# Performance work log

Hardware: AMD Instinct MI355X
Metric: run time of the kernel (lower is better)

Reference implementation:

```python
import jax, jax.numpy as jnp
import numpy as np

B, S, D, H, E, HID = 4, 1024, 768, 12, 8, 3072
DH = D // H

def _ln(x, g, b, eps=1e-5):
    m = jnp.mean(x, -1, keepdims=True)
    v = jnp.mean((x - m) ** 2, -1, keepdims=True)
    return (x - m) * jax.lax.rsqrt(v + eps) * g + b

def setup_inputs():
    key = jax.random.key(0)
    ks = jax.random.split(key, 16)
    p = lambda k, s: jax.random.normal(k, s, jnp.float32) * 0.02
    causal = jnp.triu(jnp.ones((S, S), bool), 1)  # True = masked (future)
    return {
        "x": jax.random.normal(ks[0], (B, S, D), jnp.float32),
        "mask": jnp.broadcast_to(causal, (B, S, S)),
        "ln_attn_g": jnp.ones((D,), jnp.float32), "ln_attn_b": jnp.zeros((D,), jnp.float32),
        "wq": p(ks[1], (D, D)), "bq": jnp.zeros((D,), jnp.float32),
        "wk": p(ks[2], (D, D)), "bk": jnp.zeros((D,), jnp.float32),
        "wv": p(ks[3], (D, D)), "bv": jnp.zeros((D,), jnp.float32),
        "wo": p(ks[4], (D, D)), "bo": jnp.zeros((D,), jnp.float32),
        "ln_ff_g": jnp.ones((D,), jnp.float32), "ln_ff_b": jnp.zeros((D,), jnp.float32),
        "gate_w": p(ks[5], (D, E)), "gate_b": jnp.zeros((E,), jnp.float32),
        "w1": p(ks[6], (E, D, HID)), "b1": jnp.zeros((E, HID), jnp.float32),
        "w2": p(ks[7], (E, HID, D)), "b2": jnp.zeros((E, D), jnp.float32),
        "moe_ln_g": jnp.ones((D,), jnp.float32), "moe_ln_b": jnp.zeros((D,), jnp.float32),
        "top_k": 2,
    }

def reference(x, mask, ln_attn_g, ln_attn_b, wq, bq, wk, bk, wv, bv, wo, bo,
              ln_ff_g, ln_ff_b, gate_w, gate_b, w1, b1, w2, b2,
              moe_ln_g, moe_ln_b, top_k):
    # --- pre-LN multi-head self-attention + residual ---
    a = _ln(x, ln_attn_g, ln_attn_b)
    q = (a @ wq + bq).reshape(B, S, H, DH)
    k = (a @ wk + bk).reshape(B, S, H, DH)
    v = (a @ wv + bv).reshape(B, S, H, DH)
    scores = jnp.einsum("bqhd,bkhd->bhqk", q, k) / jnp.sqrt(jnp.float32(DH))
    scores = jnp.where(mask[:, None, :, :], jnp.float32(-1e9), scores)
    probs = jax.nn.softmax(scores, axis=-1)
    ctx = jnp.einsum("bhqk,bkhd->bqhd", probs, v).reshape(B, S, D)
    x = x + (ctx @ wo + bo)
    # --- MoE positionwise FF (CustomizedMoEPositionwiseFF, pre_lnorm=False) ---
    h = _ln(x, ln_ff_g, ln_ff_b)                        # ln_ff(x) fed into ff
    logits = h @ gate_w + gate_b                        # [B,S,E] naive gate
    vals, idx = jax.lax.top_k(logits, top_k)            # [B,S,k]
    sc = jax.nn.softmax(vals, axis=-1)                  # softmax over top-k logits
    # dense all-expert compute (dropless reference for dispatch+grouped GEMM)
    e1 = jax.nn.relu(jnp.einsum("bsd,edh->bseh", h, w1) + b1)  # [B,S,E,HID]
    e2 = jnp.einsum("bseh,ehd->bsed", e1, w2) + b2             # [B,S,E,D]
    sel = jnp.take_along_axis(e2, idx[..., None], axis=2)      # [B,S,k,D]
    core = jnp.sum(sel * sc[..., None], axis=2)                # combine
    moe_out = _ln(h + core, moe_ln_g, moe_ln_b)                # post-lnorm
    return x + moe_out
```

## Files before the change

### kernel.cpp

```cpp
#include <hip/hip_runtime.h>
#include <hip/hip_bf16.h>
#include <stdint.h>

using bf16 = __hip_bfloat16;
typedef short s16x8 __attribute__((ext_vector_type(8)));
typedef float f32x4 __attribute__((ext_vector_type(4)));

#define NB 4
#define NS 1024
#define ND 768
#define NH 12
#define NE 8
#define NHID 3072
#define NTOK 4096
#define NASSIGN 8192
#define MAXCH 72
#define MAXSLOT (MAXCH * 128)

__device__ __forceinline__ float bf2f(bf16 v){ return __bfloat162float(v); }
__device__ __forceinline__ bf16 f2bf(float v){ return __float2bfloat16(v); }

__device__ __forceinline__ void gload_lds16(const bf16* g, bf16* l){
  __builtin_amdgcn_global_load_lds((const __attribute__((address_space(1))) void*)g,
                                   (__attribute__((address_space(3))) void*)l, 16, 0, 0);
}

__global__ void transpose_convert_kernel(const float* __restrict__ src, bf16* __restrict__ dst,
                                         int K, int N){
  __shared__ float tile[32][33];
  int bz = blockIdx.z;
  src += (size_t)bz * K * N;
  dst += (size_t)bz * N * K;
  int n0 = blockIdx.x * 32, k0 = blockIdx.y * 32;
  int tx = threadIdx.x & 31, ty = threadIdx.x >> 5;
  #pragma unroll
  for (int i = 0; i < 4; i++){
    int k = ty + i * 8;
    tile[k][tx] = src[(size_t)(k0 + k) * N + n0 + tx];
  }
  __syncthreads();
  #pragma unroll
  for (int i = 0; i < 4; i++){
    int n = ty + i * 8;
    dst[(size_t)(n0 + n) * K + k0 + tx] = f2bf(tile[tx][n]);
  }
}

__global__ void concat3_kernel(const float* __restrict__ a, const float* __restrict__ b,
                               const float* __restrict__ c, float* __restrict__ out){
  int i = blockIdx.x * 256 + threadIdx.x;
  if (i >= 3 * ND) return;
  float v = (i < ND) ? a[i] : (i < 2 * ND ? b[i - ND] : c[i - 2 * ND]);
  out[i] = v;
}

template<bool OF, bool OB>
__global__ void ln_kernel(const float* __restrict__ in, const float* __restrict__ g,
                          const float* __restrict__ bb, float* __restrict__ of,
                          bf16* __restrict__ ob){
  int row = blockIdx.x, t = threadIdx.x;
  const float* x = in + (size_t)row * ND;
  float v[3]; float s = 0.f, sq = 0.f;
  #pragma unroll
  for (int i = 0; i < 3; i++){ v[i] = x[t + i * 256]; s += v[i]; sq += v[i] * v[i]; }
  __shared__ float rs[4], rq[4];
  #pragma unroll
  for (int d = 32; d >= 1; d >>= 1){ s += __shfl_xor(s, d); sq += __shfl_xor(sq, d); }
  int w = t >> 6;
  if ((t & 63) == 0){ rs[w] = s; rq[w] = sq; }
  __syncthreads();
  s = rs[0] + rs[1] + rs[2] + rs[3];
  sq = rq[0] + rq[1] + rq[2] + rq[3];
  float mean = s * (1.f / ND);
  float var = sq * (1.f / ND) - mean * mean;
  float rstd = rsqrtf(var + 1e-5f);
  #pragma unroll
  for (int i = 0; i < 3; i++){
    int idx = t + i * 256;
    float y = (v[i] - mean) * rstd * g[idx] + bb[idx];
    if (OF) of[(size_t)row * ND + idx] = y;
    if (OB) ob[(size_t)row * ND + idx] = f2bf(y);
  }
}

template<int GROUP, bool GATHER, bool RELU, bool OBF, bool RESID, bool SEG>
__global__ __launch_bounds__(256, 3)
void gemm_kernel(const bf16* __restrict__ A, int ldA,
                 const bf16* __restrict__ BtB,
                 const float* __restrict__ biasB,
                 void* __restrict__ Cv, int ldC,
                 const float* __restrict__ resid,
                 int N, int K,
                 const int* __restrict__ chunk_e, const int* __restrict__ tok){
  __shared__ __align__(16) bf16 sA[2][128 * 32];
  __shared__ __align__(16) bf16 sB[2][128 * 32];

  int t = threadIdx.x;
  int lane = t & 63, wv = t >> 6;
  int c0i = wv * 128 + lane;
  int r0  = c0i >> 2;
  int kk  = (c0i & 3) * 8;
  int nt = blockIdx.x;
  int wm = (wv >> 1) * 64, wn = (wv & 1) * 64;
  int l16 = lane & 15, q4 = lane >> 4;
  int aoff[4], boff[4];
  #pragma unroll
  for (int mi = 0; mi < 4; mi++) aoff[mi] = (wm + mi * 16 + l16) * 32 + q4 * 8;
  #pragma unroll
  for (int ni = 0; ni < 4; ni++) boff[ni] = (wn + ni * 16 + l16) * 32 + q4 * 8;

  for (int g = 0; g < GROUP; g++){
    int c = blockIdx.y * GROUP + g;
    int e = 0;
    if (SEG){ e = chunk_e[c]; if (e < 0) break; }
    const bf16* Bt = SEG ? BtB + (size_t)e * N * K : BtB;
    const float* bias = SEG ? biasB + (size_t)e * N : biasB;
    size_t arow0, arow1;
    int m0 = c * 128 + r0, m1 = m0 + 16;
    if (GATHER){ arow0 = (size_t)tok[m0]; arow1 = (size_t)tok[m1]; }
    else       { arow0 = (size_t)m0;      arow1 = (size_t)m1; }
    const bf16* gA0 = A + arow0 * ldA + kk;
    const bf16* gA1 = A + arow1 * ldA + kk;
    const bf16* gB0 = Bt + (size_t)(nt * 128 + r0) * K + kk;
    const bf16* gB1 = Bt + (size_t)(nt * 128 + r0 + 16) * K + kk;

    if (g > 0) __syncthreads();

    f32x4 acc[4][4] = {};
    gload_lds16(gA0, &sA[0][(size_t)c0i * 8]);
    gload_lds16(gA1, &sA[0][(size_t)(c0i + 64) * 8]);
    gload_lds16(gB0, &sB[0][(size_t)c0i * 8]);
    gload_lds16(gB1, &sB[0][(size_t)(c0i + 64) * 8]);

    int nk = K >> 5;
    for (int ki = 0; ki < nk; ki++){
      int cur = ki & 1;
      __syncthreads();
      if (ki + 1 < nk){
        int nxt = cur ^ 1, off = (ki + 1) * 32;
        gload_lds16(gA0 + off, &sA[nxt][(size_t)c0i * 8]);
        gload_lds16(gA1 + off, &sA[nxt][(size_t)(c0i + 64) * 8]);
        gload_lds16(gB0 + off, &sB[nxt][(size_t)c0i * 8]);
        gload_lds16(gB1 + off, &sB[nxt][(size_t)(c0i + 64) * 8]);
      }
      s16x8 af[4], bfr[4];
      #pragma unroll
      for (int mi = 0; mi < 4; mi++) af[mi] = *(const s16x8*)(&sA[cur][0] + aoff[mi]);
      #pragma unroll
      for (int ni = 0; ni < 4; ni++) bfr[ni] = *(const s16x8*)(&sB[cur][0] + boff[ni]);
      #pragma unroll
      for (int mi = 0; mi < 4; mi++)
        #pragma unroll
        for (int ni = 0; ni < 4; ni++)
          acc[mi][ni] = __builtin_amdgcn_mfma_f32_16x16x32_bf16(af[mi], bfr[ni], acc[mi][ni], 0, 0, 0);
    }

    #pragma unroll
    for (int mi = 0; mi < 4; mi++){
      #pragma unroll
      for (int ni = 0; ni < 4; ni++){
        int col = nt * 128 + wn + ni * 16 + l16;
        float bv = bias[col];
        #pragma unroll
        for (int r = 0; r < 4; r++){
          size_t crow = (size_t)(c * 128 + wm + mi * 16 + q4 * 4 + r);
          float v = acc[mi][ni][r] + bv;
          if (RELU) v = fmaxf(v, 0.f);
          if (RESID) v += resid[crow * ldC + col];
          if (OBF) ((bf16*)Cv)[crow * ldC + col] = f2bf(v);
          else     ((float*)Cv)[crow * ldC + col] = v;
        }
      }
    }
  }
}

__global__ void vtrans_kernel(const bf16* __restrict__ qkv, bf16* __restrict__ vT){
  __shared__ bf16 tile[32][33];
  int bh = blockIdx.z; int b = bh / NH, h = bh % NH;
  int s0 = blockIdx.x * 32, d0 = blockIdx.y * 32;
  int tx = threadIdx.x & 31, ty = threadIdx.x >> 5;
  #pragma unroll
  for (int i = 0; i < 4; i++){
    int s = s0 + ty + i * 8;
    tile[ty + i * 8][tx] = qkv[(size_t)(b * NS + s) * 2304 + 1536 + h * 64 + d0 + tx];
  }
  __syncthreads();
  #pragma unroll
  for (int i = 0; i < 4; i++){
    int d = ty + i * 8;
    vT[((size_t)bh * 64 + d0 + d) * NS + s0 + tx] = tile[tx][d];
  }
}

#define SPAD 72
__global__ __launch_bounds__(256, 3)
void flash_attn_kernel(const bf16* __restrict__ qkv, const bf16* __restrict__ vT,
                       bf16* __restrict__ ctx){
  __shared__ __align__(16) bf16 sP[4][16 * SPAD];
  int qt = blockIdx.x, h = blockIdx.y, b = blockIdx.z;
  int t = threadIdx.x, lane = t & 63, wv = t >> 6;
  int l16 = lane & 15, q4 = lane >> 4;
  int q0 = qt * 64 + wv * 16;
  const size_t ldq = 2304;
  const bf16* qbase = qkv + (size_t)(b * NS) * ldq + h * 64;
  const bf16* kbase = qbase + 768;
  const bf16* vtb = vT + (size_t)(b * NH + h) * 64 * NS;
  bf16* sPw = &sP[wv][0];
  const f32x4 fzero = {0.f, 0.f, 0.f, 0.f};

  s16x8 qf[2];
  #pragma unroll
  for (int kh = 0; kh < 2; kh++)
    qf[kh] = *(const s16x8*)(qbase + (size_t)(q0 + l16) * ldq + kh * 32 + q4 * 8);

  f32x4 O[4] = {};
  float ms[4], ls[4];
  #pragma unroll
  for (int r = 0; r < 4; r++){ ms[r] = -1e30f; ls[r] = 0.f; }

  int kend = q0 + 16;
  for (int key0 = 0; key0 < kend; key0 += 64){
    s16x8 kf[4][2];
    #pragma unroll
    for (int ni = 0; ni < 4; ni++)
      #pragma unroll
      for (int kh = 0; kh < 2; kh++)
        kf[ni][kh] = *(const s16x8*)(kbase + (size_t)(key0 + ni * 16 + l16) * ldq + kh * 32 + q4 * 8);
    f32x4 Sf[4];
    #pragma unroll
    for (int ni = 0; ni < 4; ni++){
      Sf[ni] = __builtin_amdgcn_mfma_f32_16x16x32_bf16(qf[0], kf[ni][0], fzero, 0, 0, 0);
      Sf[ni] = __builtin_amdgcn_mfma_f32_16x16x32_bf16(qf[1], kf[ni][1], Sf[ni], 0, 0, 0);
    }
    s16x8 vf[4][2];
    #pragma unroll
    for (int dt = 0; dt < 4; dt++)
      #pragma unroll
      for (int kh = 0; kh < 2; kh++)
        vf[dt][kh] = *(const s16x8*)(vtb + (size_t)(dt * 16 + l16) * NS + key0 + kh * 32 + q4 * 8);

    bool need_mask = (key0 + 63 >= q0);
    #pragma unroll
    for (int r = 0; r < 4; r++){
      int qrow = q0 + q4 * 4 + r;
      float sv[4];
      #pragma unroll
      for (int ni = 0; ni < 4; ni++){
        sv[ni] = Sf[ni][r] * 0.125f;
        if (need_mask && (key0 + ni * 16 + l16 > qrow)) sv[ni] = -1e30f;
      }
      float mx = fmaxf(fmaxf(sv[0], sv[1]), fmaxf(sv[2], sv[3]));
      #pragma unroll
      for (int d = 8; d >= 1; d >>= 1) mx = fmaxf(mx, __shfl_xor(mx, d));
      float mnew = fmaxf(ms[r], mx);
      float alpha = __expf(ms[r] - mnew);
      float p[4], psum = 0.f;
      #pragma unroll
      for (int ni = 0; ni < 4; ni++){ p[ni] = __expf(sv[ni] - mnew); psum += p[ni]; }
      #pragma unroll
      for (int d = 8; d >= 1; d >>= 1) psum += __shfl_xor(psum, d);
      ls[r] = ls[r] * alpha + psum;
      ms[r] = mnew;
      #pragma unroll
      for (int dt = 0; dt < 4; dt++) O[dt][r] *= alpha;
      int prow = q4 * 4 + r;
      #pragma unroll
      for (int ni = 0; ni < 4; ni++)
        sPw[prow * SPAD + ni * 16 + l16] = f2bf(p[ni]);
    }
    s16x8 pf[2];
    #pragma unroll
    for (int kh = 0; kh < 2; kh++)
      pf[kh] = *(const s16x8*)(sPw + l16 * SPAD + kh * 32 + q4 * 8);
    #pragma unroll
    for (int dt = 0; dt < 4; dt++){
      O[dt] = __builtin_amdgcn_mfma_f32_16x16x32_bf16(pf[0], vf[dt][0], O[dt], 0, 0, 0);
      O[dt] = __builtin_amdgcn_mfma_f32_16x16x32_bf16(pf[1], vf[dt][1], O[dt], 0, 0, 0);
    }
  }

  #pragma unroll
  for (int r = 0; r < 4; r++){
    float inv = 1.f / ls[r];
    int qrow = q0 + q4 * 4 + r;
    #pragma unroll
    for (int dt = 0; dt < 4; dt++)
      ctx[(size_t)(b * NS + qrow) * ND + h * 64 + dt * 16 + l16] = f2bf(O[dt][r] * inv);
  }
}

__global__ __launch_bounds__(256)
void gate_kernel(const float* __restrict__ h, const float* __restrict__ gw,
                 const float* __restrict__ gb, int* __restrict__ ridx,
                 float* __restrict__ rw, int* __restrict__ counts){
  __shared__ float sgw[NE * ND];
  __shared__ int scnt[NE];
  int t = threadIdx.x;
  if (t < NE) scnt[t] = 0;
  for (int idx = t; idx < ND * NE; idx += 256){
    int i = idx >> 3, e = idx & 7;
    sgw[e * ND + i] = gw[idx];
  }
  __syncthreads();
  int lane = t & 63, wv = t >> 6;
  for (int it = 0; it < 8; it++){
    int tok = blockIdx.x * 32 + it * 4 + wv;
    const float* hr = h + (size_t)tok * ND;
    float acc[NE] = {};
    #pragma unroll
    for (int ii = 0; ii < 12; ii++){
      int i = lane + ii * 64;
      float hv = hr[i];
      #pragma unroll
      for (int e = 0; e < NE; e++) acc[e] += hv * sgw[e * ND + i];
    }
    #pragma unroll
    for (int e = 0; e < NE; e++)
      #pragma unroll
      for (int d = 32; d >= 1; d >>= 1) acc[e] += __shfl_xor(acc[e], d);
    if (lane == 0){
      float v0 = -1e30f, v1 = -1e30f; int i0 = 0, i1 = 0;
      #pragma unroll
      for (int e = 0; e < NE; e++){
        float v = acc[e] + gb[e];
        if (v > v0){ v1 = v0; i1 = i0; v0 = v; i0 = e; }
        else if (v > v1){ v1 = v; i1 = e; }
      }
      float w0 = 1.f / (1.f + __expf(v1 - v0));
      ridx[tok * 2] = i0; ridx[tok * 2 + 1] = i1;
      rw[tok * 2] = w0;  rw[tok * 2 + 1] = 1.f - w0;
      atomicAdd(&scnt[i0], 1);
      atomicAdd(&scnt[i1], 1);
    }
  }
  __syncthreads();
  if (t < NE) atomicAdd(&counts[t], scnt[t]);
}

__global__ void scan_kernel(const int* __restrict__ counts, int* __restrict__ poff,
                            int* __restrict__ chunk_e, int* __restrict__ tok_list){
  int t = threadIdx.x;
  for (int i = t; i < MAXSLOT; i += 256) tok_list[i] = 0;
  if (t == 0){
    int s = 0, c = 0;
    for (int e = 0; e < NE; e++){
      poff[e] = s;
      int nch = (counts[e] + 127) >> 7;
      for (int i = 0; i < nch; i++) chunk_e[c++] = e;
      s += nch << 7;
    }
    for (; c < MAXCH; c++) chunk_e[c] = -1;
  }
}

__global__ void scatter_kernel(const int* __restrict__ ridx, const int* __restrict__ poff,
                               int* __restrict__ cursor, int* __restrict__ tok_list,
                               int* __restrict__ slot_of){
  int tk = blockIdx.x * 256 + threadIdx.x;
  int lane = threadIdx.x & 63;
  int e = ridx[tk];
  unsigned long long lmask = (lane == 63) ? ~0ull : ((1ull << (lane + 1)) - 1);
  lmask >>= 1; lmask <<= 1; lmask = (1ull << lane) - 1;
  int slot = 0;
  #pragma unroll
  for (int ee = 0; ee < NE; ee++){
    unsigned long long mask = __ballot(e == ee);
    if (mask == 0ull) continue;
    int leader = __ffsll((unsigned long long)mask) - 1;
    int base = 0;
    if (lane == leader) base = atomicAdd(&cursor[ee], __popcll(mask));
    base = __shfl(base, leader);
    if (e == ee) slot = poff[ee] + base + __popcll(mask & lmask);
  }
  tok_list[slot] = tk >> 1;
  slot_of[tk] = slot;
}

__global__ void combine_kernel(const bf16* __restrict__ e2, const int* __restrict__ slot_of,
                               const float* __restrict__ rw, const float* __restrict__ hf,
                               const float* __restrict__ attn_x, const float* __restrict__ g,
                               const float* __restrict__ bb, float* __restrict__ out){
  int row = blockIdx.x, t = threadIdx.x;
  int sl0 = slot_of[row * 2], sl1 = slot_of[row * 2 + 1];
  float w0 = rw[row * 2], w1 = rw[row * 2 + 1];
  const bf16* r0 = e2 + (size_t)sl0 * ND;
  const bf16* r1 = e2 + (size_t)sl1 * ND;
  const float* hr = hf + (size_t)row * ND;
  float v[3]; float s = 0.f, sq = 0.f;
  #pragma unroll
  for (int i = 0; i < 3; i++){
    int idx = t + i * 256;
    float c = w0 * bf2f(r0[idx]) + w1 * bf2f(r1[idx]);
    float xv = hr[idx] + c;
    v[i] = xv; s += xv; sq += xv * xv;
  }
  __shared__ float rs[4], rq[4];
  #pragma unroll
  for (int d = 32; d >= 1; d >>= 1){ s += __shfl_xor(s, d); sq += __shfl_xor(sq, d); }
  int w = t >> 6;
  if ((t & 63) == 0){ rs[w] = s; rq[w] = sq; }
  __syncthreads();
  s = rs[0] + rs[1] + rs[2] + rs[3];
  sq = rq[0] + rq[1] + rq[2] + rq[3];
  float mean = s * (1.f / ND);
  float var = sq * (1.f / ND) - mean * mean;
  float rstd = rsqrtf(var + 1e-5f);
  #pragma unroll
  for (int i = 0; i < 3; i++){
    int idx = t + i * 256;
    float y = (v[i] - mean) * rstd * g[idx] + bb[idx];
    out[(size_t)row * ND + idx] = attn_x[(size_t)row * ND + idx] + y;
  }
}

extern "C" void kernel_launch(void* const* d_in, const int* in_sizes, int n_in,
                              void* d_out, int out_size, void* d_ws, size_t ws_size,
                              hipStream_t stream){
  const float* x        = (const float*)d_in[0];
  const float* ln_att_g = (const float*)d_in[2];
  const float* ln_att_b = (const float*)d_in[3];
  const float* wq = (const float*)d_in[4];  const float* bq = (const float*)d_in[5];
  const float* wk = (const float*)d_in[6];  const float* bk = (const float*)d_in[7];
  const float* wv = (const float*)d_in[8];  const float* bv = (const float*)d_in[9];
  const float* wo = (const float*)d_in[10]; const float* bo = (const float*)d_in[11];
  const float* ln_ff_g = (const float*)d_in[12];
  const float* ln_ff_b = (const float*)d_in[13];
  const float* gate_w  = (const float*)d_in[14];
  const float* gate_b  = (const float*)d_in[15];
  const float* w1 = (const float*)d_in[16]; const float* b1 = (const float*)d_in[17];
  const float* w2 = (const float*)d_in[18]; const float* b2 = (const float*)d_in[19];
  const float* moe_g = (const float*)d_in[20];
  const float* moe_b = (const float*)d_in[21];

  uint8_t* p = (uint8_t*)d_ws;
  auto alloc = [&](size_t bytes) -> void* {
    void* r = (void*)p;
    p += (bytes + 255) & ~(size_t)255;
    return r;
  };
  bf16* wqkv_t  = (bf16*)alloc((size_t)2304 * 768 * 2);
  bf16* wo_t    = (bf16*)alloc((size_t)768 * 768 * 2);
  bf16* w1_t    = (bf16*)alloc((size_t)NE * NHID * ND * 2);
  bf16* w2_t    = (bf16*)alloc((size_t)NE * ND * NHID * 2);
  float* bias_qkv = (float*)alloc(2304 * 4);
  bf16* a_bf    = (bf16*)alloc((size_t)NTOK * ND * 2);
  bf16* qkv     = (bf16*)alloc((size_t)NTOK * 2304 * 2);
  bf16* vT      = (bf16*)alloc((size_t)NB * NH * 64 * NS * 2);
  bf16* ctx     = (bf16*)alloc((size_t)NTOK * ND * 2);
  float* attn_x = (float*)alloc((size_t)NTOK * ND * 4);
  float* h_f    = (float*)alloc((size_t)NTOK * ND * 4);
  bf16* h_b     = (bf16*)alloc((size_t)NTOK * ND * 2);
  int*  ridx    = (int*)alloc(NASSIGN * 4);
  float* rwt    = (float*)alloc(NASSIGN * 4);
  int* counts   = (int*)alloc(NE * 4);
  int* poff     = (int*)alloc(NE * 4);
  int* cursor   = (int*)alloc(NE * 4);
  int* chunk_e  = (int*)alloc(MAXCH * 4);
  int* tok_list = (int*)alloc(MAXSLOT * 4);
  int* slot_of  = (int*)alloc(NASSIGN * 4);
  bf16* e1      = (bf16*)alloc((size_t)MAXSLOT * NHID * 2);
  bf16* e2      = (bf16*)alloc((size_t)MAXSLOT * ND * 2);

  hipMemsetAsync(counts, 0, NE * 4, stream);
  hipMemsetAsync(cursor, 0, NE * 4, stream);

  transpose_convert_kernel<<<dim3(24, 24, 1), 256, 0, stream>>>(wq, wqkv_t, 768, 768);
  transpose_convert_kernel<<<dim3(24, 24, 1), 256, 0, stream>>>(wk, wqkv_t + (size_t)768 * 768, 768, 768);
  transpose_convert_kernel<<<dim3(24, 24, 1), 256, 0, stream>>>(wv, wqkv_t + (size_t)1536 * 768, 768, 768);
  transpose_convert_kernel<<<dim3(24, 24, 1), 256, 0, stream>>>(wo, wo_t, 768, 768);
  transpose_convert_kernel<<<dim3(96, 24, NE), 256, 0, stream>>>(w1, w1_t, 768, 3072);
  transpose_convert_kernel<<<dim3(24, 96, NE), 256, 0, stream>>>(w2, w2_t, 3072, 768);
  concat3_kernel<<<dim3(9), 256, 0, stream>>>(bq, bk, bv, bias_qkv);

  ln_kernel<false, true><<<dim3(NTOK), 256, 0, stream>>>(x, ln_att_g, ln_att_b, nullptr, a_bf);
  gemm_kernel<2, false, false, true, false, false><<<dim3(18, 16), 256, 0, stream>>>(
      a_bf, ND, wqkv_t, bias_qkv, qkv, 2304, nullptr, 2304, ND, nullptr, nullptr);
  vtrans_kernel<<<dim3(32, 2, NB * NH), 256, 0, stream>>>(qkv, vT);
  flash_attn_kernel<<<dim3(16, NH, NB), 256, 0, stream>>>(qkv, vT, ctx);
  gemm_kernel<1, false, false, false, true, false><<<dim3(6, 32), 256, 0, stream>>>(
      ctx, ND, wo_t, bo, attn_x, ND, x, ND, ND, nullptr, nullptr);

  ln_kernel<true, true><<<dim3(NTOK), 256, 0, stream>>>(attn_x, ln_ff_g, ln_ff_b, h_f, h_b);
  gate_kernel<<<dim3(NTOK / 32), 256, 0, stream>>>(h_f, gate_w, gate_b, ridx, rwt, counts);
  scan_kernel<<<dim3(1), 256, 0, stream>>>(counts, poff, chunk_e, tok_list);
  scatter_kernel<<<dim3(NASSIGN / 256), 256, 0, stream>>>(ridx, poff, cursor, tok_list, slot_of);
  gemm_kernel<2, true, true, true, false, true><<<dim3(24, 36), 256, 0, stream>>>(
      h_b, ND, w1_t, b1, e1, NHID, nullptr, NHID, ND, chunk_e, tok_list);
  gemm_kernel<1, false, false, true, false, true><<<dim3(6, 72), 256, 0, stream>>>(
      e1, NHID, w2_t, b2, e2, ND, nullptr, ND, NHID, chunk_e, nullptr);
  combine_kernel<<<dim3(NTOK), 256, 0, stream>>>(e2, slot_of, rwt, h_f, attn_x, moe_g, moe_b,
                                                 (float*)d_out);
}
```

Baseline: 610.0 us.

## Stage K/V tiles through double-buffered LDS and schedule heavy causal blocks first

The flash attention kernel now loads shared 64x64 K and V tiles into double-buffered LDS with async global-to-LDS loads and an XOR swizzle, so all four waves share one copy instead of each wave loading from global memory. The next tile's load is issued while the current one is computed. The grid is flattened and query tiles run in reverse order, so the longest causal blocks start first for better load balance. This adds a block-wide barrier per tile and 32KB of LDS, which may lower occupancy. Waves whose rows are already finished now idle through the extra tiles.

After: 553.9 us. 9.2% less time.

```diff
diff --git a/kernel.cpp b/kernel.cpp
--- a/kernel.cpp
+++ b/kernel.cpp
@@ -197,15 +197,20 @@
 __global__ __launch_bounds__(256, 3)
 void flash_attn_kernel(const bf16* __restrict__ qkv, const bf16* __restrict__ vT,
                        bf16* __restrict__ ctx){
+  __shared__ __align__(16) bf16 sK[2][64 * 64];
+  __shared__ __align__(16) bf16 sV[2][64 * 64];
   __shared__ __align__(16) bf16 sP[4][16 * SPAD];
-  int qt = blockIdx.x, h = blockIdx.y, b = blockIdx.z;
+  int id = blockIdx.x;
+  int bh = id % 48;
+  int qt = 15 - (id / 48);
+  int b = bh / NH, h = bh % NH;
   int t = threadIdx.x, lane = t & 63, wv = t >> 6;
   int l16 = lane & 15, q4 = lane >> 4;
   int q0 = qt * 64 + wv * 16;
   const size_t ldq = 2304;
   const bf16* qbase = qkv + (size_t)(b * NS) * ldq + h * 64;
   const bf16* kbase = qbase + 768;
-  const bf16* vtb = vT + (size_t)(b * NH + h) * 64 * NS;
+  const bf16* vtb = vT + (size_t)bh * 64 * NS;
   bf16* sPw = &sP[wv][0];
   const f32x4 fzero = {0.f, 0.f, 0.f, 0.f};
 
@@ -219,64 +224,85 @@
   #pragma unroll
   for (int r = 0; r < 4; r++){ ms[r] = -1e30f; ls[r] = 0.f; }
 
-  int kend = q0 + 16;
-  for (int key0 = 0; key0 < kend; key0 += 64){
-    s16x8 kf[4][2];
+  int sub = lane >> 3, rawc = lane & 7;
+  auto stage = [&](int buf, int key0){
     #pragma unroll
-    for (int ni = 0; ni < 4; ni++)
+    for (int i = 0; i < 2; i++){
+      int rk = wv * 8 + sub + i * 32;
+      int cs = (rawc ^ (rk & 7)) * 8;
+      gload_lds16(kbase + (size_t)(key0 + rk) * ldq + cs, &sK[buf][wv * 512 + i * 2048]);
+      gload_lds16(vtb + (size_t)rk * NS + key0 + cs,      &sV[buf][wv * 512 + i * 2048]);
+    }
+  };
+
+  int ntiles = qt + 1;
+  stage(0, 0);
+  for (int ti = 0; ti < ntiles; ti++){
+    int cur = ti & 1, key0 = ti * 64;
+    __syncthreads();
+    if (ti + 1 < ntiles) stage(cur ^ 1, (ti + 1) * 64);
+    if (key0 <= q0 + 15){
+      const bf16* sKc = &sK[cur][0];
+      const bf16* sVc = &sV[cur][0];
+      s16x8 kf[4][2], vf[4][2];
+      #pragma unroll
+      for (int ni = 0; ni < 4; ni++){
+        int krow = ni * 16 + l16;
+        #pragma unroll
+        for (int kh = 0; kh < 2; kh++)
+          kf[ni][kh] = *(const s16x8*)(sKc + krow * 64 + (((kh * 4 + q4) ^ (krow & 7)) * 8));
+      }
+      #pragma unroll
+      for (int dt = 0; dt < 4; dt++){
+        int vrow = dt * 16 + l16;
+        #pragma unroll
+        for (int kh = 0; kh < 2; kh++)
+          vf[dt][kh] = *(const s16x8*)(sVc + vrow * 64 + (((kh * 4 + q4) ^ (vrow & 7)) * 8));
+      }
+      f32x4 Sf[4];
+      #pragma unroll
+      for (int ni = 0; ni < 4; ni++){
+        Sf[ni] = __builtin_amdgcn_mfma_f32_16x16x32_bf16(qf[0], kf[ni][0], fzero, 0, 0, 0);
+        Sf[ni] = __builtin_amdgcn_mfma_f32_16x16x32_bf16(qf[1], kf[ni][1], Sf[ni], 0, 0, 0);
+      }
+      bool need_mask = (key0 + 63 >= q0);
+      #pragma unroll
+      for (int r = 0; r < 4; r++){
+        int qrow = q0 + q4 * 4 + r;
+        float sv[4];
+        #pragma unroll
+        for (int ni = 0; ni < 4; ni++){
+          sv[ni] = Sf[ni][r] * 0.125f;
+          if (need_mask && (key0 + ni * 16 + l16 > qrow)) sv[ni] = -1e30f;
+        }
+        float mx = fmaxf(fmaxf(sv[0], sv[1]), fmaxf(sv[2], sv[3]));
+        #pragma unroll
+        for (int d = 8; d >= 1; d >>= 1) mx = fmaxf(mx, __shfl_xor(mx, d));
+        float mnew = fmaxf(ms[r], mx);
+        float alpha = __expf(ms[r] - mnew);
+        float p[4], psum = 0.f;
+        #pragma unroll
+        for (int ni = 0; ni < 4; ni++){ p[ni] = __expf(sv[ni] - mnew); psum += p[ni]; }
+        #pragma unroll
+        for (int d = 8; d >= 1; d >>= 1) psum += __shfl_xor(psum, d);
+        ls[r] = ls[r] * alpha + psum;
+        ms[r] = mnew;
+        #pragma unroll
+        for (int dt = 0; dt < 4; dt++) O[dt][r] *= alpha;
+        int prow = q4 * 4 + r;
+        #pragma unroll
+        for (int ni = 0; ni < 4; ni++)
+          sPw[prow * SPAD + ni * 16 + l16] = f2bf(p[ni]);
+      }
+      s16x8 pf[2];
       #pragma unroll
       for (int kh = 0; kh < 2; kh++)
-        kf[ni][kh] = *(const s16x8*)(kbase + (size_t)(key0 + ni * 16 + l16) * ldq + kh * 32 + q4 * 8);
-    f32x4 Sf[4];
-    #pragma unroll
-    for (int ni = 0; ni < 4; ni++){
-      Sf[ni] = __builtin_amdgcn_mfma_f32_16x16x32_bf16(qf[0], kf[ni][0], fzero, 0, 0, 0);
-      Sf[ni] = __builtin_amdgcn_mfma_f32_16x16x32_bf16(qf[1], kf[ni][1], Sf[ni], 0, 0, 0);
-    }
-    s16x8 vf[4][2];
-    #pragma unroll
-    for (int dt = 0; dt < 4; dt++)
-      #pragma unroll
-      for (int kh = 0; kh < 2; kh++)
-        vf[dt][kh] = *(const s16x8*)(vtb + (size_t)(dt * 16 + l16) * NS + key0 + kh * 32 + q4 * 8);
-
-    bool need_mask = (key0 + 63 >= q0);
-    #pragma unroll
-    for (int r = 0; r < 4; r++){
-      int qrow = q0 + q4 * 4 + r;
-      float sv[4];
-      #pragma unroll
-      for (int ni = 0; ni < 4; ni++){
-        sv[ni] = Sf[ni][r] * 0.125f;
-        if (need_mask && (key0 + ni * 16 + l16 > qrow)) sv[ni] = -1e30f;
-      }
-      float mx = fmaxf(fmaxf(sv[0], sv[1]), fmaxf(sv[2], sv[3]));
-      #pragma unroll
-      for (int d = 8; d >= 1; d >>= 1) mx = fmaxf(mx, __shfl_xor(mx, d));
-      float mnew = fmaxf(ms[r], mx);
-      float alpha = __expf(ms[r] - mnew);
-      float p[4], psum = 0.f;
-      #pragma unroll
-      for (int ni = 0; ni < 4; ni++){ p[ni] = __expf(sv[ni] - mnew); psum += p[ni]; }
-      #pragma unroll
-      for (int d = 8; d >= 1; d >>= 1) psum += __shfl_xor(psum, d);
-      ls[r] = ls[r] * alpha + psum;
-      ms[r] = mnew;
-      #pragma unroll
-      for (int dt = 0; dt < 4; dt++) O[dt][r] *= alpha;
-      int prow = q4 * 4 + r;
-      #pragma unroll
-      for (int ni = 0; ni < 4; ni++)
-        sPw[prow * SPAD + ni * 16 + l16] = f2bf(p[ni]);
-    }
-    s16x8 pf[2];
-    #pragma unroll
-    for (int kh = 0; kh < 2; kh++)
-      pf[kh] = *(const s16x8*)(sPw + l16 * SPAD + kh * 32 + q4 * 8);
-    #pragma unroll
-    for (int dt = 0; dt < 4; dt++){
-      O[dt] = __builtin_amdgcn_mfma_f32_16x16x32_bf16(pf[0], vf[dt][0], O[dt], 0, 0, 0);
-      O[dt] = __builtin_amdgcn_mfma_f32_16x16x32_bf16(pf[1], vf[dt][1], O[dt], 0, 0, 0);
+        pf[kh] = *(const s16x8*)(sPw + l16 * SPAD + kh * 32 + q4 * 8);
+      #pragma unroll
+      for (int dt = 0; dt < 4; dt++){
+        O[dt] = __builtin_amdgcn_mfma_f32_16x16x32_bf16(pf[0], vf[dt][0], O[dt], 0, 0, 0);
+        O[dt] = __builtin_amdgcn_mfma_f32_16x16x32_bf16(pf[1], vf[dt][1], O[dt], 0, 0, 0);
+      }
     }
   }
 
@@ -360,8 +386,7 @@
   int tk = blockIdx.x * 256 + threadIdx.x;
   int lane = threadIdx.x & 63;
   int e = ridx[tk];
-  unsigned long long lmask = (lane == 63) ? ~0ull : ((1ull << (lane + 1)) - 1);
-  lmask >>= 1; lmask <<= 1; lmask = (1ull << lane) - 1;
+  unsigned long long lmask = (1ull << lane) - 1;
   int slot = 0;
   #pragma unroll
   for (int ee = 0; ee < NE; ee++){
@@ -477,7 +502,7 @@
   gemm_kernel<2, false, false, true, false, false><<<dim3(18, 16), 256, 0, stream>>>(
       a_bf, ND, wqkv_t, bias_qkv, qkv, 2304, nullptr, 2304, ND, nullptr, nullptr);
   vtrans_kernel<<<dim3(32, 2, NB * NH), 256, 0, stream>>>(qkv, vT);
-  flash_attn_kernel<<<dim3(16, NH, NB), 256, 0, stream>>>(qkv, vT, ctx);
+  flash_attn_kernel<<<dim3(768), 256, 0, stream>>>(qkv, vT, ctx);
   gemm_kernel<1, false, false, false, true, false><<<dim3(6, 32), 256, 0, stream>>>(
       ctx, ND, wo_t, bo, attn_x, ND, x, ND, ND, nullptr, nullptr);
 
```
